# Kernel tuning notes

Measured on AMD Instinct MI355X. Metric: run time of the kernel, lower is better.

Reference implementation:

```python
import jax, jax.numpy as jnp
import numpy as np
from jax import lax


def _conv3d(x, w, b, circular=False):
    # x: (B,C,D,H,W), w: (O,I,kd,kh,kw)
    if circular:
        x = jnp.pad(x, ((0, 0), (0, 0), (1, 1), (1, 1), (1, 1)), mode='wrap')
    y = lax.conv_general_dilated(x, w, (1, 1, 1), 'VALID',
                                 dimension_numbers=('NCDHW', 'OIDHW', 'NCDHW'))
    return y + b[None, :, None, None, None]


def _inorm(x):
    # InstanceNorm3d, affine=False, eps=1e-5, biased variance over spatial dims
    mu = jnp.mean(x, axis=(2, 3, 4), keepdims=True)
    var = jnp.var(x, axis=(2, 3, 4), keepdims=True)
    return (x - mu) * lax.rsqrt(var + 1e-5)


def _gelu(x):
    return jax.nn.gelu(x, approximate=False)


def _r6_to_matrix(r6):
    eps = 1e-7
    v1 = r6[..., :3]
    v1 = v1 / (jnp.linalg.norm(v1, axis=-1, keepdims=True) + eps)
    v2 = r6[..., 3:]
    v2 = v2 - jnp.sum(v2 * v1, -1, keepdims=True) * v1
    v2 = v2 / (jnp.linalg.norm(v2, axis=-1, keepdims=True) + eps)
    v3 = jnp.cross(v1, v2)
    det = jnp.linalg.det(jnp.stack([v1, v2, v3], axis=-2))
    v3 = jnp.where(det[..., None] < 0, -v3, v3)
    return jnp.stack([v1, v2, v3], axis=-2)


def _ensure_matrix(R):
    def fnorm(v):
        return v / jnp.maximum(jnp.linalg.norm(v, axis=-1, keepdims=True), 1e-12)
    v1 = fnorm(R[..., 0, :] + 1e-6)
    v2 = R[..., 1, :]
    v2 = fnorm(v2 - jnp.sum(v2 * v1, -1, keepdims=True) * v1 + 1e-6)
    v3 = jnp.cross(v1, v2)
    det = jnp.linalg.det(jnp.stack([v1, v2, v3], axis=-2))
    v3 = jnp.where(det[..., None] < 0, -v3, v3)
    Rn = jnp.stack([v1, v2, v3], axis=-2)
    Rt = jnp.swapaxes(Rn, -2, -1)
    return 0.5 * (Rn + Rt @ Rn @ Rt)


def _rotate(X, R):
    # X: (bd, nh, L, hd); R: (nh, 3, 3). Pads hd to a multiple of 3, rotates
    # each 3-vector group by R^T-on-the-right (X_rot = X @ R^T).
    hd = X.shape[-1]
    pad = (-hd) % 3
    Xp = jnp.pad(X, ((0, 0), (0, 0), (0, 0), (0, pad))) if pad else X
    nv = Xp.shape[-1] // 3
    Xr = Xp.reshape(Xp.shape[:-1] + (nv, 3))
    Y = jnp.einsum('bhlvi,hji->bhlvj', Xr, R).reshape(Xp.shape)
    return Y[..., :hd] if pad else Y


def _forward(x, pos_emb, qkv_w, qkv_b, lp_w1, lp_b1, lp_w2, lp_b2,
             mod_w1, mod_b1, mod_w2, mod_b2, pa_w, pa_b,
             proj_w, proj_b, pos_bias_w, pos_bias_b,
             A_d, A_h, A_w, R_d, R_h, R_w, t_d, t_h, t_w):
    B, C, D, H, W = x.shape
    nh = pa_w.shape[0]
    hd = C // nh
    scale = hd ** -0.5

    # PositionalProcessing (identical for all three axial passes)
    lf = _conv3d(pos_emb, lp_w1, lp_b1, circular=True)
    lf = _conv3d(_gelu(_inorm(lf)), lp_w2, lp_b2)
    m = _conv3d(lf, mod_w1, mod_b1)
    m = jax.nn.sigmoid(_conv3d(_gelu(_inorm(m)), mod_w2, mod_b2))
    x_mod = x * m                                   # (B,C,D,H,W)
    pa = _gelu(_inorm(_conv3d(pos_emb, pa_w, pa_b)))  # (B,nh,D,H,W)

    def axial(comp, perm, inv_perm, A, R, t):
        xp = jnp.transpose(x_mod, perm)             # (B, a, b, C, L)
        Bp, a, b, _, L = xp.shape
        bd = Bp * a * b
        xf = jnp.swapaxes(xp.reshape(bd, C, L), 1, 2)  # (bd, L, C)
        qkv = (xf @ qkv_w.T + qkv_b).reshape(bd, L, 3, nh, hd)
        qkv = jnp.transpose(qkv, (2, 0, 3, 1, 4))
        q, k, v = qkv[0], qkv[1], qkv[2]
        R_qk = _r6_to_matrix(A[0].astype(jnp.float32))  # (nh,3,3), same for all bd
        R_v = _ensure_matrix(R[0])                      # (nh,3,3)
        q_r, k_r, v_r = _rotate(q, R_qk), _rotate(k, R_qk), _rotate(v, R_v)
        # axis positions: linspace on one coordinate component
        pos = jnp.zeros((L, 3), x.dtype).at[:, comp].set(jnp.linspace(-1.0, 1.0, L))
        pos_t = pos[None] + t[0]                        # (nh, L, 3)
        rel = pos_t[:, :, None, :] - pos_t[:, None, :, :]  # (nh, L, L, 3)
        bias = jnp.einsum('hqkc,c->hqk', rel, pos_bias_w[0]) + pos_bias_b[0]
        pa_p = jnp.transpose(pa, perm).reshape(bd, nh, L)
        attn = jnp.einsum('bhqd,bhkd->bhqk', q_r, k_r) * scale
        attn = jax.nn.softmax(attn + pa_p[..., None] + bias[None], axis=-1)
        out = jnp.einsum('bhqk,bhkd->bhqd', attn, v_r)
        out = jnp.transpose(out, (0, 2, 1, 3)).reshape(Bp, a, b, L, C)
        return jnp.transpose(out, inv_perm)             # back to (B,C,D,H,W)

    out = (axial(2, (0, 3, 4, 1, 2), (0, 4, 3, 1, 2), A_d, R_d, t_d)
           + axial(1, (0, 2, 4, 1, 3), (0, 4, 1, 3, 2), A_h, R_h, t_h)
           + axial(0, (0, 2, 3, 1, 4), (0, 4, 1, 2, 3), A_w, R_w, t_w))
    return jnp.einsum('oc,bcdhw->bodhw', proj_w[:, :, 0, 0, 0], out) + proj_b[None, :, None, None, None]


def setup_inputs() -> dict:
    key = jax.random.key(0)
    B, C, D, H, W, nh = 2, 128, 32, 32, 32, 8
    ks = jax.random.split(key, 24)

    def n(k, shape, s=0.05):
        return (jax.random.normal(k, shape) * s).astype(jnp.float32)

    def r6(k):
        k1, k2 = jax.random.split(k)
        v1 = jax.random.normal(k1, (1, nh, 3))
        v1 = v1 / jnp.linalg.norm(v1, axis=-1, keepdims=True)
        v2 = jax.random.normal(k2, (1, nh, 3))
        v2 = v2 - jnp.sum(v2 * v1, -1, keepdims=True) * v1
        v2 = v2 / jnp.linalg.norm(v2, axis=-1, keepdims=True)
        return jnp.concatenate([v1, v2], -1).astype(jnp.float32)

    eye = jnp.broadcast_to(jnp.eye(3, dtype=jnp.float32), (1, nh, 3, 3))
    return {
        'x': jax.random.normal(ks[0], (B, C, D, H, W), jnp.float32),
        'pos_emb': jax.random.normal(ks[1], (B, C, D, H, W), jnp.float32),
        'qkv_w': n(ks[2], (3 * C, C)), 'qkv_b': n(ks[3], (3 * C,)),
        'lp_w1': n(ks[4], (C, C, 3, 3, 3), 0.02), 'lp_b1': n(ks[5], (C,)),
        'lp_w2': n(ks[6], (C, C, 1, 1, 1)), 'lp_b2': n(ks[7], (C,)),
        'mod_w1': n(ks[8], (C, C, 1, 1, 1)), 'mod_b1': n(ks[9], (C,)),
        'mod_w2': n(ks[10], (C, C, 1, 1, 1)), 'mod_b2': n(ks[11], (C,)),
        'pa_w': n(ks[12], (nh, C, 1, 1, 1)), 'pa_b': n(ks[13], (nh,)),
        'proj_w': n(ks[14], (C, C, 1, 1, 1)), 'proj_b': n(ks[15], (C,)),
        'pos_bias_w': n(ks[16], (1, 3), 0.5), 'pos_bias_b': n(ks[17], (1,)),
        'A_d': r6(ks[18]), 'A_h': r6(ks[19]), 'A_w': r6(ks[20]),
        'R_d': eye, 'R_h': eye, 'R_w': eye,
        't_d': n(ks[21], (1, nh, 1, 3), 0.01),
        't_h': n(ks[22], (1, nh, 1, 3), 0.01),
        't_w': n(ks[23], (1, nh, 1, 3), 0.01),
    }


def reference(x, pos_emb, qkv_w, qkv_b, lp_w1, lp_b1, lp_w2, lp_b2,
              mod_w1, mod_b1, mod_w2, mod_b2, pa_w, pa_b,
              proj_w, proj_b, pos_bias_w, pos_bias_b,
              A_d, A_h, A_w, R_d, R_h, R_w, t_d, t_h, t_w):
    return _forward(x, pos_emb, qkv_w, qkv_b, lp_w1, lp_b1, lp_w2, lp_b2,
                    mod_w1, mod_b1, mod_w2, mod_b2, pa_w, pa_b,
                    proj_w, proj_b, pos_bias_w, pos_bias_b,
                    A_d, A_h, A_w, R_d, R_h, R_w, t_d, t_h, t_w)
```

## Files before the change

kernel.cpp:

```cpp
#include <hip/hip_runtime.h>
#include <cstdint>
#include <cstddef>


#define NTOK 65536
#define SPAT 32768

#define WS_R0     0ull
#define WS_A0     0ull
#define WS_A1     4194304ull
#define WS_MPREB  8388608ull
#define WS_A2     8388608ull
#define WS_XTOKB  12582912ull
#define WS_INT    16777216ull
#define WS_QKVH   20971520ull
#define WS_CONVP  33554432ull
#define WS_QKVP   33775616ull
#define WS_WCP    33800192ull
#define WS_MODW2P 33808384ull
#define WS_PROJP  33816576ull
#define WS_BC     33824768ull
#define WS_RBUF   33824896ull
#define WS_PS     33825328ull
#define WS_PSS    33956400ull
#define WS_MU1    34087472ull
#define WS_RS1    34087728ull
#define WS_MU2    34087984ull
#define WS_RS2    34088240ull

typedef __attribute__((ext_vector_type(8))) short short8;
typedef __attribute__((ext_vector_type(4))) float f32x4;
typedef __attribute__((ext_vector_type(16))) float f32x16;

__device__ __forceinline__ float gelu_f(float x) {
  return 0.5f * x * (1.0f + erff(x * 0.70710678118654752f));
}
__device__ __forceinline__ float sigmoid_f(float x) {
  return 1.0f / (1.0f + expf(-x));
}
__device__ __forceinline__ unsigned short f2bf(float x) {
  unsigned int u = __float_as_uint(x);
  unsigned int r = u + 0x7fffu + ((u >> 16) & 1u);
  return (unsigned short)(r >> 16);
}
__device__ __forceinline__ float bf2f(unsigned short u) {
  return __uint_as_float(((unsigned int)u) << 16);
}
__device__ __forceinline__ void bf16x16_load(const unsigned short* p, float* f) {
  const uint4 a = *(const uint4*)p;
  const uint4 b = *(const uint4*)(p + 8);
  const unsigned int w[8] = {a.x, a.y, a.z, a.w, b.x, b.y, b.z, b.w};
  #pragma unroll
  for (int i = 0; i < 8; ++i) {
    f[2 * i] = __uint_as_float(w[i] << 16);
    f[2 * i + 1] = __uint_as_float(w[i] & 0xffff0000u);
  }
}
__device__ __forceinline__ void gload_lds16(const void* g, void* l) {
  __builtin_amdgcn_global_load_lds(
      (const __attribute__((address_space(1))) unsigned int*)g,
      (__attribute__((address_space(3))) unsigned int*)l, 16, 0, 0);
}
__device__ __forceinline__ float dot3(const float* a, const float* b) {
  return a[0] * b[0] + a[1] * b[1] + a[2] * b[2];
}
__device__ __forceinline__ void cross3(const float* a, const float* b, float* c) {
  c[0] = a[1] * b[2] - a[2] * b[1];
  c[1] = a[2] * b[0] - a[0] * b[2];
  c[2] = a[0] * b[1] - a[1] * b[0];
}

__device__ void r6_to_matrix(const float* r6, float* R) {
  float v1[3] = {r6[0], r6[1], r6[2]};
  float n1 = sqrtf(dot3(v1, v1));
  float inv1 = 1.0f / (n1 + 1e-7f);
  v1[0] *= inv1; v1[1] *= inv1; v1[2] *= inv1;
  float v2[3] = {r6[3], r6[4], r6[5]};
  float d = dot3(v2, v1);
  v2[0] -= d * v1[0]; v2[1] -= d * v1[1]; v2[2] -= d * v1[2];
  float n2 = sqrtf(dot3(v2, v2));
  float inv2 = 1.0f / (n2 + 1e-7f);
  v2[0] *= inv2; v2[1] *= inv2; v2[2] *= inv2;
  float v3[3]; cross3(v1, v2, v3);
  float cx[3]; cross3(v2, v3, cx);
  float det = dot3(v1, cx);
  if (det < 0.0f) { v3[0] = -v3[0]; v3[1] = -v3[1]; v3[2] = -v3[2]; }
  R[0] = v1[0]; R[1] = v1[1]; R[2] = v1[2];
  R[3] = v2[0]; R[4] = v2[1]; R[5] = v2[2];
  R[6] = v3[0]; R[7] = v3[1]; R[8] = v3[2];
}

__device__ void ensure_matrix(const float* Rin, float* Ro) {
  float a[3] = {Rin[0] + 1e-6f, Rin[1] + 1e-6f, Rin[2] + 1e-6f};
  float na = fmaxf(sqrtf(dot3(a, a)), 1e-12f);
  float v1[3] = {a[0] / na, a[1] / na, a[2] / na};
  float b0[3] = {Rin[3], Rin[4], Rin[5]};
  float d = dot3(b0, v1);
  float bb[3] = {b0[0] - d * v1[0] + 1e-6f, b0[1] - d * v1[1] + 1e-6f, b0[2] - d * v1[2] + 1e-6f};
  float nb = fmaxf(sqrtf(dot3(bb, bb)), 1e-12f);
  float v2[3] = {bb[0] / nb, bb[1] / nb, bb[2] / nb};
  float v3[3]; cross3(v1, v2, v3);
  float cx[3]; cross3(v2, v3, cx);
  float det = dot3(v1, cx);
  if (det < 0.0f) { v3[0] = -v3[0]; v3[1] = -v3[1]; v3[2] = -v3[2]; }
  float Rn[9] = {v1[0], v1[1], v1[2], v2[0], v2[1], v2[2], v3[0], v3[1], v3[2]};
  float T1[9], T2[9];
  for (int i = 0; i < 3; ++i)
    for (int j = 0; j < 3; ++j) {
      float s = 0.f;
      for (int k = 0; k < 3; ++k) s += Rn[k * 3 + i] * Rn[k * 3 + j];
      T1[i * 3 + j] = s;
    }
  for (int i = 0; i < 3; ++i)
    for (int j = 0; j < 3; ++j) {
      float s = 0.f;
      for (int k = 0; k < 3; ++k) s += T1[i * 3 + k] * Rn[j * 3 + k];
      T2[i * 3 + j] = s;
    }
  for (int i = 0; i < 9; ++i) Ro[i] = 0.5f * (Rn[i] + T2[i]);
}

__device__ __forceinline__ void rot16(const float* R, const float* x, float* y) {
  #pragma unroll
  for (int g = 0; g < 5; ++g) {
    float a = x[3 * g], b = x[3 * g + 1], c = x[3 * g + 2];
    y[3 * g + 0] = R[0] * a + R[1] * b + R[2] * c;
    y[3 * g + 1] = R[3] * a + R[4] * b + R[5] * c;
    y[3 * g + 2] = R[6] * a + R[7] * b + R[8] * c;
  }
  y[15] = R[0] * x[15];
}

__global__ __launch_bounds__(256) void prep_transpose_kernel(
    const float* __restrict__ lp_w1, const float* __restrict__ qkv_w,
    const float* __restrict__ mod_w1, const float* __restrict__ lp_w2,
    const float* __restrict__ lp_b2, const float* __restrict__ mod_b1,
    const float* __restrict__ mod_w2, const float* __restrict__ proj_w,
    const float* __restrict__ Ad, const float* __restrict__ Ah,
    const float* __restrict__ Aw, const float* __restrict__ Rd,
    const float* __restrict__ Rh, const float* __restrict__ Rw,
    const float* __restrict__ x, const float* __restrict__ pe,
    unsigned short* __restrict__ convP, unsigned short* __restrict__ qkvP,
    unsigned short* __restrict__ WcP, unsigned short* __restrict__ modw2P,
    unsigned short* __restrict__ projP, float* __restrict__ bc,
    float* __restrict__ Rbuf, unsigned short* __restrict__ xtokb,
    unsigned short* __restrict__ inT) {
  __shared__ float lds[32][132];
  if (blockIdx.x < 256) {
    int gid = blockIdx.x * 256 + threadIdx.x;
    for (int f = gid; f < 442368; f += 65536) {
      int e = f & 7;
      int co = (f >> 3) & 127;
      int rest = f >> 10;
      int l4 = rest & 3;
      int ks = (rest >> 2) & 3;
      int dxt = rest >> 4;
      int dx = dxt % 3;
      int tap = dxt / 3;
      int dz = tap / 3, dy = tap % 3;
      int ci = ks * 32 + l4 * 8 + e;
      convP[f] = f2bf(lp_w1[(co * 128 + ci) * 27 + dz * 9 + dy * 3 + dx]);
    }
    if (gid < 49152) qkvP[gid] = f2bf(qkv_w[gid]);
    if (gid < 16384) {
      modw2P[gid] = f2bf(mod_w2[gid]);
      projP[gid] = f2bf(proj_w[gid]);
      int o = gid >> 7, i = gid & 127;
      float s = 0.f;
      for (int c = 0; c < 128; ++c) s += mod_w1[o * 128 + c] * lp_w2[c * 128 + i];
      WcP[gid] = f2bf(s);
    }
    if (gid < 128) {
      float s = 0.f;
      for (int c = 0; c < 128; ++c) s += mod_w1[gid * 128 + c] * lp_b2[c];
      bc[gid] = s + mod_b1[gid];
    }
    if (blockIdx.x == 0 && threadIdx.x >= 224 && threadIdx.x < 248) {
      int tid = threadIdx.x - 224;
      int ax = tid >> 3, h = tid & 7;
      const float* A = (ax == 0) ? Ad : ((ax == 1) ? Ah : Aw);
      const float* R = (ax == 0) ? Rd : ((ax == 1) ? Rh : Rw);
      float Rq[9], Rv[9];
      r6_to_matrix(A + h * 6, Rq);
      ensure_matrix(R + h * 9, Rv);
      float* dst = Rbuf + (ax * 8 + h) * 18;
      for (int i = 0; i < 9; ++i) { dst[i] = Rq[i]; dst[9 + i] = Rv[i]; }
    }
    return;
  }
  int blk = blockIdx.x - 256;
  int b = blk >> 10;
  int dh = blk & 1023;
  int tid = threadIdx.x;
  size_t planebase = ((size_t)b << 22) + ((size_t)dh << 5);
  size_t tb = ((size_t)blk) << 5;
  #pragma unroll
  for (int r = 0; r < 16; ++r) {
    int idx = r * 256 + tid;
    int ci = idx >> 5, w = idx & 31;
    lds[w][ci] = x[planebase + ((size_t)ci << 15) + w];
  }
  __syncthreads();
  #pragma unroll
  for (int r = 0; r < 16; ++r) {
    int idx = r * 256 + tid;
    int w = idx >> 7, ci = idx & 127;
    xtokb[(tb + w) * 128 + ci] = f2bf(lds[w][ci]);
  }
  __syncthreads();
  #pragma unroll
  for (int r = 0; r < 16; ++r) {
    int idx = r * 256 + tid;
    int ci = idx >> 5, w = idx & 31;
    lds[w][ci] = pe[planebase + ((size_t)ci << 15) + w];
  }
  __syncthreads();
  #pragma unroll
  for (int r = 0; r < 16; ++r) {
    int idx = r * 256 + tid;
    int w = idx >> 7, ci = idx & 127;
    inT[(tb + w) * 128 + ci] = f2bf(lds[w][ci]);
  }
}

__global__ __launch_bounds__(256, 4) void conv_mfma_kernel(
    const unsigned short* __restrict__ inT, const unsigned short* __restrict__ Bp,
    const float* __restrict__ b1, unsigned short* __restrict__ out,
    float* __restrict__ ps, float* __restrict__ pss) {
  __shared__ unsigned short Als[16384];
  __shared__ float sumb[128];
  __shared__ float sqb[128];
  const int orig = blockIdx.x;
  const int blk = ((orig & 7) << 7) + (orig >> 3);
  const int b = blk >> 9, d = (blk >> 4) & 31, hg = blk & 15;
  const int h0 = hg << 1;
  const int tid = threadIdx.x;
  const int lane = tid & 63;
  const int wid = tid >> 6;
  const int l15 = lane & 15, l4 = lane >> 4;

  f32x4 acc[4][2];
  #pragma unroll
  for (int mt = 0; mt < 4; ++mt)
    #pragma unroll
    for (int nt = 0; nt < 2; ++nt)
      #pragma unroll
      for (int r = 0; r < 4; ++r) acc[mt][nt][r] = 0.f;

  int mw[4], mhh[4];
  #pragma unroll
  for (int mt = 0; mt < 4; ++mt) {
    int m = mt * 16 + l15;
    mhh[mt] = m >> 5;
    mw[mt] = m & 31;
  }
  const size_t tokbase = ((size_t)b << 15) + ((size_t)d << 10) + ((size_t)h0 << 5);

  auto stage = [&](int dz) {
    const int zr = (d + dz + 31) & 31;
    #pragma unroll
    for (int p = 0; p < 8; ++p) {
      const int g = p * 256 + tid;
      const int tok = g >> 4, gi = g & 15;
      const int r = tok >> 5, w = tok & 31;
      const int yr = (h0 + r + 31) & 31;
      const size_t srcbyte = ((((size_t)b << 15) + ((size_t)zr << 10) + ((size_t)yr << 5) + w) << 8)
                             + (size_t)((gi ^ (w & 7)) << 4);
      gload_lds16((const char*)inT + srcbyte, (char*)Als + (size_t)g * 16);
    }
  };

  auto compute = [&](int dz) {
    #pragma unroll
    for (int dy = 0; dy < 3; ++dy) {
      const int tap = dz * 3 + dy;
      #pragma unroll
      for (int dx = 0; dx < 3; ++dx) {
        int abase[4], asw[4];
        #pragma unroll
        for (int mt = 0; mt < 4; ++mt) {
          const int wsft = (mw[mt] + dx + 31) & 31;
          const int stok = (mhh[mt] + dy) * 32 + wsft;
          abase[mt] = stok * 256;
          asw[mt] = (wsft & 7) << 4;
        }
        #pragma unroll
        for (int ks = 0; ks < 4; ++ks) {
          const int k2 = (ks * 32 + l4 * 8) * 2;
          const int bbase = (((tap * 3 + dx) * 4 + ks) * 4 + l4) * 1024;
          short8 afr[4], bfr[2];
          #pragma unroll
          for (int nt = 0; nt < 2; ++nt) {
            const int co = wid * 32 + nt * 16 + l15;
            bfr[nt] = *(const short8*)(Bp + bbase + co * 8);
          }
          #pragma unroll
          for (int mt = 0; mt < 4; ++mt)
            afr[mt] = *(const short8*)((const char*)Als + abase[mt] + (k2 ^ asw[mt]));
          __builtin_amdgcn_s_setprio(1);
          #pragma unroll
          for (int mt = 0; mt < 4; ++mt)
            #pragma unroll
            for (int nt = 0; nt < 2; ++nt)
              acc[mt][nt] = __builtin_amdgcn_mfma_f32_16x16x32_bf16(afr[mt], bfr[nt],
                                                                    acc[mt][nt], 0, 0, 0);
          __builtin_amdgcn_s_setprio(0);
        }
      }
    }
  };

  for (int dz = 0; dz < 3; ++dz) {
    stage(dz);
    __syncthreads();
    compute(dz);
    if (dz < 2) __syncthreads();
  }

  #pragma unroll
  for (int nt = 0; nt < 2; ++nt) {
    const int co = wid * 32 + nt * 16 + l15;
    const float bias = b1[co];
    float s = 0.f, q = 0.f;
    #pragma unroll
    for (int mt = 0; mt < 4; ++mt) {
      #pragma unroll
      for (int r = 0; r < 4; ++r) {
        const int m = mt * 16 + l4 * 4 + r;
        const float v = acc[mt][nt][r] + bias;
        out[(tokbase + m) * 128 + co] = f2bf(v);
        s += v; q += v * v;
      }
    }
    s += __shfl_xor(s, 16); s += __shfl_xor(s, 32);
    q += __shfl_xor(q, 16); q += __shfl_xor(q, 32);
    if (l4 == 0) { sumb[co] = s; sqb[co] = q; }
  }
  __syncthreads();
  if (tid < 128) {
    ps[blk * 128 + tid] = sumb[tid];
    pss[blk * 128 + tid] = sqb[tid];
  }
}

__global__ __launch_bounds__(64) void stats_final_kernel(
    const float* __restrict__ ps, const float* __restrict__ pss,
    float* __restrict__ mu, float* __restrict__ rs, int nb) {
  const int pair = blockIdx.x;
  const int b = pair >> 7, c = pair & 127;
  const int lane = threadIdx.x;
  float s = 0.f, ss = 0.f;
  for (int j = lane; j < nb; j += 64) {
    const int idx = ((b * nb + j) << 7) + c;
    s += ps[idx];
    ss += pss[idx];
  }
  #pragma unroll
  for (int o = 32; o > 0; o >>= 1) {
    s += __shfl_xor(s, o);
    ss += __shfl_xor(ss, o);
  }
  if (lane == 0) {
    float m = s * (1.0f / 32768.0f);
    float v = ss * (1.0f / 32768.0f) - m * m;
    mu[pair] = m;
    rs[pair] = rsqrtf(v + 1e-5f);
  }
}

template <int PRE, int AB16, int POST, int STATS>
__global__ __launch_bounds__(256) void gemm_mfma_kernel(
    const void* __restrict__ Avoid, const unsigned short* __restrict__ Wp,
    const float* __restrict__ bias, void* __restrict__ Yvoid, int O,
    const float* __restrict__ mu, const float* __restrict__ rs,
    const unsigned short* __restrict__ xtb, float* __restrict__ ps,
    float* __restrict__ pss) {
  __shared__ float sumb[128][2];
  __shared__ float sqb[128][2];
  const int tid = threadIdx.x;
  const int lane = tid & 63, wid = tid >> 6;
  const int wm = wid >> 1, wn = wid & 1;
  const int l15 = lane & 15, l4 = lane >> 4;
  const int og = blockIdx.x * 128;
  const int t0 = blockIdx.y * 128;
  const int bidx = t0 >> 15;
  const float* Af = (const float*)Avoid;
  const unsigned short* Ab = (const unsigned short*)Avoid;
  float* Yf = (float*)Yvoid;
  unsigned short* Yb = (unsigned short*)Yvoid;

  f32x4 acc[4][4];
  #pragma unroll
  for (int mt = 0; mt < 4; ++mt)
    #pragma unroll
    for (int nt = 0; nt < 4; ++nt)
      #pragma unroll
      for (int r = 0; r < 4; ++r) acc[mt][nt][r] = 0.f;

  #pragma unroll
  for (int ks = 0; ks < 4; ++ks) {
    const int kb = ks * 32 + l4 * 8;
    short8 a[4], bfr[4];
    float4 m0, m1, r0, r1;
    if constexpr (PRE == 1) {
      m0 = *(const float4*)(mu + bidx * 128 + kb);
      m1 = *(const float4*)(mu + bidx * 128 + kb + 4);
      r0 = *(const float4*)(rs + bidx * 128 + kb);
      r1 = *(const float4*)(rs + bidx * 128 + kb + 4);
    }
    #pragma unroll
    for (int mt = 0; mt < 4; ++mt) {
      const int tok = t0 + wm * 64 + mt * 16 + l15;
      float v[16];
      bool have = false;
      if constexpr (AB16 == 1) {
        if constexpr (PRE == 1) {
          bf16x16_load(Ab + (size_t)tok * 128 + kb, v);
          have = true;
        } else {
          a[mt] = *(const short8*)(Ab + (size_t)tok * 128 + kb);
        }
      } else {
        const float* ap = Af + (size_t)tok * 128 + kb;
        float4 v0 = *(const float4*)ap;
        float4 v1 = *(const float4*)(ap + 4);
        v[0] = v0.x; v[1] = v0.y; v[2] = v0.z; v[3] = v0.w;
        v[4] = v1.x; v[5] = v1.y; v[6] = v1.z; v[7] = v1.w;
        have = true;
      }
      if (have) {
        if constexpr (PRE == 1) {
          const float mm[8] = {m0.x, m0.y, m0.z, m0.w, m1.x, m1.y, m1.z, m1.w};
          const float rr[8] = {r0.x, r0.y, r0.z, r0.w, r1.x, r1.y, r1.z, r1.w};
          #pragma unroll
          for (int j = 0; j < 8; ++j) v[j] = gelu_f((v[j] - mm[j]) * rr[j]);
        }
        short8 t;
        #pragma unroll
        for (int j = 0; j < 8; ++j) t[j] = (short)f2bf(v[j]);
        a[mt] = t;
      }
    }
    #pragma unroll
    for (int nt = 0; nt < 4; ++nt) {
      const int o = og + wn * 64 + nt * 16 + l15;
      bfr[nt] = *(const short8*)(Wp + (size_t)o * 128 + kb);
    }
    #pragma unroll
    for (int mt = 0; mt < 4; ++mt)
      #pragma unroll
      for (int nt = 0; nt < 4; ++nt)
        acc[mt][nt] = __builtin_amdgcn_mfma_f32_16x16x32_bf16(a[mt], bfr[nt], acc[mt][nt], 0, 0, 0);
  }

  #pragma unroll
  for (int nt = 0; nt < 4; ++nt) {
    const int o = og + wn * 64 + nt * 16 + l15;
    const float bb = bias[o];
    float s = 0.f, q = 0.f;
    #pragma unroll
    for (int mt = 0; mt < 4; ++mt) {
      #pragma unroll
      for (int r = 0; r < 4; ++r) {
        const int t = t0 + wm * 64 + mt * 16 + l4 * 4 + r;
        const float v = acc[mt][nt][r] + bb;
        if constexpr (POST == 0) {
          Yf[(size_t)t * O + o] = v;
        } else if constexpr (POST == 2) {
          Yb[(size_t)t * O + o] = f2bf(v);
        }
        if constexpr (STATS) { s += v; q += v * v; }
      }
    }
    if constexpr (STATS) {
      s += __shfl_xor(s, 16); s += __shfl_xor(s, 32);
      q += __shfl_xor(q, 16); q += __shfl_xor(q, 32);
      if (l4 == 0) { sumb[o - og][wm] = s; sqb[o - og][wm] = q; }
    }
  }
  if constexpr (STATS) {
    __syncthreads();
    if (tid < 128) {
      ps[blockIdx.y * 128 + tid] = sumb[tid][0] + sumb[tid][1];
      pss[blockIdx.y * 128 + tid] = sqb[tid][0] + sqb[tid][1];
    }
  }
}

__global__ __launch_bounds__(256) void gateqkv_mfma_kernel(
    const unsigned short* __restrict__ mpreb, const unsigned short* __restrict__ modw2P,
    const float* __restrict__ mod_b2, const unsigned short* __restrict__ xtb,
    const unsigned short* __restrict__ qkvP, const float* __restrict__ qkv_b,
    unsigned short* __restrict__ qkvt, const float* __restrict__ mu,
    const float* __restrict__ rs) {
  __shared__ char xm[32768];
  const int tid = threadIdx.x;
  const int lane = tid & 63, wid = tid >> 6;
  const int wm = wid >> 1, wn = wid & 1;
  const int l15 = lane & 15, l4 = lane >> 4;
  const int t0 = blockIdx.x * 128;
  const int bidx = t0 >> 15;

  f32x4 acc[4][4];
  #pragma unroll
  for (int mt = 0; mt < 4; ++mt)
    #pragma unroll
    for (int nt = 0; nt < 4; ++nt)
      #pragma unroll
      for (int r = 0; r < 4; ++r) acc[mt][nt][r] = 0.f;

  #pragma unroll
  for (int ks = 0; ks < 4; ++ks) {
    const int kb = ks * 32 + l4 * 8;
    short8 a[4], bfr[4];
    const float4 m0 = *(const float4*)(mu + bidx * 128 + kb);
    const float4 m1 = *(const float4*)(mu + bidx * 128 + kb + 4);
    const float4 r0 = *(const float4*)(rs + bidx * 128 + kb);
    const float4 r1 = *(const float4*)(rs + bidx * 128 + kb + 4);
    const float mm[8] = {m0.x, m0.y, m0.z, m0.w, m1.x, m1.y, m1.z, m1.w};
    const float rr[8] = {r0.x, r0.y, r0.z, r0.w, r1.x, r1.y, r1.z, r1.w};
    #pragma unroll
    for (int mt = 0; mt < 4; ++mt) {
      const int tok = t0 + wm * 64 + mt * 16 + l15;
      float v[16];
      bf16x16_load(mpreb + (size_t)tok * 128 + kb, v);
      short8 t;
      #pragma unroll
      for (int j = 0; j < 8; ++j) t[j] = (short)f2bf(gelu_f((v[j] - mm[j]) * rr[j]));
      a[mt] = t;
    }
    #pragma unroll
    for (int nt = 0; nt < 4; ++nt) {
      const int o = wn * 64 + nt * 16 + l15;
      bfr[nt] = *(const short8*)(modw2P + (size_t)o * 128 + kb);
    }
    #pragma unroll
    for (int mt = 0; mt < 4; ++mt)
      #pragma unroll
      for (int nt = 0; nt < 4; ++nt)
        acc[mt][nt] = __builtin_amdgcn_mfma_f32_16x16x32_bf16(a[mt], bfr[nt], acc[mt][nt], 0, 0, 0);
  }
  #pragma unroll
  for (int nt = 0; nt < 4; ++nt) {
    const int o = wn * 64 + nt * 16 + l15;
    const float bb = mod_b2[o];
    #pragma unroll
    for (int mt = 0; mt < 4; ++mt) {
      #pragma unroll
      for (int r = 0; r < 4; ++r) {
        const int tl = wm * 64 + mt * 16 + l4 * 4 + r;
        const int t = t0 + tl;
        const float v = sigmoid_f(acc[mt][nt][r] + bb) * bf2f(xtb[(size_t)t * 128 + o]);
        *(unsigned short*)(xm + tl * 256 + ((o * 2) ^ ((tl & 7) << 4))) = f2bf(v);
      }
    }
  }
  __syncthreads();

  for (int c = 0; c < 3; ++c) {
    #pragma unroll
    for (int mt = 0; mt < 4; ++mt)
      #pragma unroll
      for (int nt = 0; nt < 4; ++nt)
        #pragma unroll
        for (int r = 0; r < 4; ++r) acc[mt][nt][r] = 0.f;
    #pragma unroll
    for (int ks = 0; ks < 4; ++ks) {
      const int kb = ks * 32 + l4 * 8;
      short8 a[4], bfr[4];
      #pragma unroll
      for (int mt = 0; mt < 4; ++mt) {
        const int tl = wm * 64 + mt * 16 + l15;
        a[mt] = *(const short8*)(xm + tl * 256 + ((kb * 2) ^ ((tl & 7) << 4)));
      }
      #pragma unroll
      for (int nt = 0; nt < 4; ++nt) {
        const int o = c * 128 + wn * 64 + nt * 16 + l15;
        bfr[nt] = *(const short8*)(qkvP + (size_t)o * 128 + kb);
      }
      #pragma unroll
      for (int mt = 0; mt < 4; ++mt)
        #pragma unroll
        for (int nt = 0; nt < 4; ++nt)
          acc[mt][nt] = __builtin_amdgcn_mfma_f32_16x16x32_bf16(a[mt], bfr[nt], acc[mt][nt], 0, 0, 0);
    }
    #pragma unroll
    for (int nt = 0; nt < 4; ++nt) {
      const int o = c * 128 + wn * 64 + nt * 16 + l15;
      const float bb = qkv_b[o];
      const int hsub = (o & 127) >> 4, ch = o & 15;
      #pragma unroll
      for (int mt = 0; mt < 4; ++mt) {
        #pragma unroll
        for (int r = 0; r < 4; ++r) {
          const int t = t0 + wm * 64 + mt * 16 + l4 * 4 + r;
          qkvt[(size_t)t * 384 + hsub * 48 + c * 16 + ch] = f2bf(acc[mt][nt][r] + bb);
        }
      }
    }
  }
}

__global__ __launch_bounds__(256) void proj_mfma_kernel(
    const unsigned short* __restrict__ A0b, const unsigned short* __restrict__ A1b,
    const unsigned short* __restrict__ A2b, const unsigned short* __restrict__ Wp,
    const float* __restrict__ bias, float* __restrict__ out) {
  const int tid = threadIdx.x;
  const int lane = tid & 63, wid = tid >> 6;
  const int wm = wid >> 1, wn = wid & 1;
  const int l15 = lane & 15, l4 = lane >> 4;
  const int t0 = blockIdx.x * 128;

  f32x4 acc[4][4];
  #pragma unroll
  for (int mt = 0; mt < 4; ++mt)
    #pragma unroll
    for (int nt = 0; nt < 4; ++nt)
      #pragma unroll
      for (int r = 0; r < 4; ++r) acc[mt][nt][r] = 0.f;

  #pragma unroll
  for (int ks = 0; ks < 4; ++ks) {
    const int kb = ks * 32 + l4 * 8;
    short8 a[4], bfr[4];
    #pragma unroll
    for (int mt = 0; mt < 4; ++mt) {
      const int o = wm * 64 + mt * 16 + l15;
      a[mt] = *(const short8*)(Wp + (size_t)o * 128 + kb);
    }
    #pragma unroll
    for (int nt = 0; nt < 4; ++nt) {
      const int tok = t0 + wn * 64 + nt * 16 + l15;
      const size_t off = (size_t)tok * 128 + kb;
      short8 s0 = *(const short8*)(A0b + off);
      short8 s1 = *(const short8*)(A1b + off);
      short8 s2 = *(const short8*)(A2b + off);
      short8 r;
      #pragma unroll
      for (int i = 0; i < 8; ++i) {
        float f = bf2f((unsigned short)s0[i]) + bf2f((unsigned short)s1[i]) +
                  bf2f((unsigned short)s2[i]);
        r[i] = (short)f2bf(f);
      }
      bfr[nt] = r;
    }
    #pragma unroll
    for (int mt = 0; mt < 4; ++mt)
      #pragma unroll
      for (int nt = 0; nt < 4; ++nt)
        acc[mt][nt] = __builtin_amdgcn_mfma_f32_16x16x32_bf16(a[mt], bfr[nt], acc[mt][nt], 0, 0, 0);
  }

  #pragma unroll
  for (int nt = 0; nt < 4; ++nt) {
    const int tok = t0 + wn * 64 + nt * 16 + l15;
    const int dhw = tok & 32767, bB = tok >> 15;
    #pragma unroll
    for (int mt = 0; mt < 4; ++mt) {
      #pragma unroll
      for (int r = 0; r < 4; ++r) {
        const int o = wm * 64 + mt * 16 + l4 * 4 + r;
        out[((size_t)(bB * 128 + o) << 15) + dhw] = acc[mt][nt][r] + bias[o];
      }
    }
  }
}

__global__ __launch_bounds__(512) void attn_mfma_kernel(
    const unsigned short* __restrict__ qkvt, const float* __restrict__ Rbuf,
    const float* __restrict__ pbw, unsigned short* __restrict__ a0,
    unsigned short* __restrict__ a1, unsigned short* __restrict__ a2) {
  __shared__ unsigned short rows[32 * 392];
  __shared__ unsigned short Vt[8][16 * 40];
  __shared__ float Ot[8][32 * 20];
  const int axial = blockIdx.y;
  const int seq = blockIdx.x;
  unsigned short* dstbuf = (axial == 0) ? a0 : ((axial == 1) ? a1 : a2);
  const int tid = threadIdx.x;
  const int lane = tid & 63, head = tid >> 6;
  const int tok = lane & 31, hi = lane >> 5;
  const int b = seq >> 10, rem = seq & 1023;
  const int u = rem >> 5, v = rem & 31;
  int base, stride, comp;
  if (axial == 0)      { base = (b << 15) + (u << 5) + v;         stride = 1024; comp = 2; }
  else if (axial == 1) { base = (b << 15) + (u << 10) + v;        stride = 32;   comp = 1; }
  else                 { base = (b << 15) + (u << 10) + (v << 5); stride = 1;    comp = 0; }

  #pragma unroll
  for (int p = 0; p < 3; ++p) {
    const int c = p * 512 + tid;
    const int r = c / 48, cw = c - r * 48;
    const size_t src = ((size_t)base + (size_t)r * stride) * 384 + (size_t)cw * 8;
    *(uint4*)((char*)rows + r * 784 + cw * 16) = *(const uint4*)(qkvt + src);
  }
  __syncthreads();

  const float* Rp = Rbuf + (axial * 8 + head) * 18;
  const float rq00 = fabsf(Rp[0]);
  const unsigned short* myrow = rows + tok * 392 + head * 48;
  short8 aq = *(const short8*)(myrow + hi * 8);
  short8 ak = *(const short8*)(myrow + 16 + hi * 8);
  short8 av = *(const short8*)(myrow + 32 + hi * 8);
  if (hi) {
    aq[7] = (short)f2bf(bf2f((unsigned short)aq[7]) * rq00);
    ak[7] = (short)f2bf(bf2f((unsigned short)ak[7]) * rq00);
  }
  #pragma unroll
  for (int e = 0; e < 8; ++e) Vt[head][(hi * 8 + e) * 40 + tok] = (unsigned short)av[e];

  f32x16 sacc;
  #pragma unroll
  for (int r = 0; r < 16; ++r) sacc[r] = 0.f;
  sacc = __builtin_amdgcn_mfma_f32_32x32x16_bf16(ak, aq, sacc, 0, 0, 0);
  const float wb = pbw[comp];
  float p[16];
  float mmax = -1e30f;
  #pragma unroll
  for (int r = 0; r < 16; ++r) {
    const int kk = (r & 3) + 4 * hi + 8 * (r >> 2);
    const float lin = -1.0f + (2.0f / 31.0f) * (float)kk;
    p[r] = sacc[r] * 0.25f - lin * wb;
    mmax = fmaxf(mmax, p[r]);
  }
  mmax = fmaxf(mmax, __shfl_xor(mmax, 32));
  float sum = 0.f;
  #pragma unroll
  for (int r = 0; r < 16; ++r) { p[r] = expf(p[r] - mmax); sum += p[r]; }
  sum += __shfl_xor(sum, 32);
  const float inv = 1.0f / sum;
  #pragma unroll
  for (int r = 0; r < 16; ++r) p[r] *= inv;
  unsigned pk[8], sw[8];
  #pragma unroll
  for (int j = 0; j < 8; ++j) {
    unsigned r_;
    asm("v_cvt_pk_bf16_f32 %0, %1, %2" : "=v"(r_) : "v"(p[2 * j]), "v"(p[2 * j + 1]));
    pk[j] = r_;
  }
  #pragma unroll
  for (int j = 0; j < 8; ++j) sw[j] = (unsigned)__shfl_xor((int)pk[j], 32);
  uint4 Fu, Gu;
  Fu.x = hi ? sw[2] : pk[0];
  Fu.y = hi ? sw[3] : pk[1];
  Fu.z = hi ? pk[2] : sw[0];
  Fu.w = hi ? pk[3] : sw[1];
  Gu.x = hi ? sw[6] : pk[4];
  Gu.y = hi ? sw[7] : pk[5];
  Gu.z = hi ? pk[6] : sw[4];
  Gu.w = hi ? pk[7] : sw[5];
  short8 Pf = *(short8*)&Fu;
  short8 Pg = *(short8*)&Gu;
  const unsigned short* vrow = Vt[head] + (tok & 15) * 40;
  short8 Bv0 = *(const short8*)(vrow + hi * 8);
  short8 Bv1 = *(const short8*)(vrow + 16 + hi * 8);
  f32x16 oacc;
  #pragma unroll
  for (int r = 0; r < 16; ++r) oacc[r] = 0.f;
  oacc = __builtin_amdgcn_mfma_f32_32x32x16_bf16(Pf, Bv0, oacc, 0, 0, 0);
  oacc = __builtin_amdgcn_mfma_f32_32x32x16_bf16(Pg, Bv1, oacc, 0, 0, 0);
  if (tok < 16) {
    #pragma unroll
    for (int r = 0; r < 16; ++r) {
      const int q = (r & 3) + 4 * hi + 8 * (r >> 2);
      Ot[head][q * 20 + tok] = oacc[r];
    }
  }
  if (lane < 32) {
    float o16[16], y16[16], Rv[9];
    #pragma unroll
    for (int j = 0; j < 16; ++j) o16[j] = Ot[head][lane * 20 + j];
    #pragma unroll
    for (int i = 0; i < 9; ++i) Rv[i] = Rp[9 + i];
    rot16(Rv, o16, y16);
    unsigned outw[8];
    #pragma unroll
    for (int j = 0; j < 8; ++j)
      outw[j] = ((unsigned)f2bf(y16[2 * j + 1]) << 16) | (unsigned)f2bf(y16[2 * j]);
    const size_t t2 = (size_t)base + (size_t)lane * stride;
    unsigned short* dst = dstbuf + t2 * 128 + head * 16;
    uint4 o0 = {outw[0], outw[1], outw[2], outw[3]};
    uint4 o1 = {outw[4], outw[5], outw[6], outw[7]};
    *(uint4*)dst = o0;
    *(uint4*)(dst + 8) = o1;
  }
}

extern "C" void kernel_launch(void* const* d_in, const int* in_sizes, int n_in,
                              void* d_out, int out_size, void* d_ws, size_t ws_size,
                              hipStream_t stream) {
  const float* x       = (const float*)d_in[0];
  const float* pos_emb = (const float*)d_in[1];
  const float* qkv_w   = (const float*)d_in[2];
  const float* qkv_b   = (const float*)d_in[3];
  const float* lp_w1   = (const float*)d_in[4];
  const float* lp_b1   = (const float*)d_in[5];
  const float* lp_w2   = (const float*)d_in[6];
  const float* lp_b2   = (const float*)d_in[7];
  const float* mod_w1  = (const float*)d_in[8];
  const float* mod_b1  = (const float*)d_in[9];
  const float* mod_w2  = (const float*)d_in[10];
  const float* mod_b2  = (const float*)d_in[11];
  const float* proj_w  = (const float*)d_in[14];
  const float* proj_b  = (const float*)d_in[15];
  const float* pbw     = (const float*)d_in[16];
  const float* Ad      = (const float*)d_in[18];
  const float* Ah      = (const float*)d_in[19];
  const float* Aw      = (const float*)d_in[20];
  const float* Rd      = (const float*)d_in[21];
  const float* Rh      = (const float*)d_in[22];
  const float* Rw      = (const float*)d_in[23];

  float* ws = (float*)d_ws;
  unsigned short* lfb    = (unsigned short*)(ws + WS_R0);
  unsigned short* A0b    = (unsigned short*)(ws + WS_A0);
  unsigned short* A1b    = (unsigned short*)(ws + WS_A1);
  unsigned short* A2b    = (unsigned short*)(ws + WS_A2);
  unsigned short* mpreb  = (unsigned short*)(ws + WS_MPREB);
  unsigned short* xtokb  = (unsigned short*)(ws + WS_XTOKB);
  unsigned short* inT    = (unsigned short*)(ws + WS_INT);
  unsigned short* qkvt   = (unsigned short*)(ws + WS_QKVH);
  unsigned short* convP  = (unsigned short*)(ws + WS_CONVP);
  unsigned short* qkvP   = (unsigned short*)(ws + WS_QKVP);
  unsigned short* WcP    = (unsigned short*)(ws + WS_WCP);
  unsigned short* modw2P = (unsigned short*)(ws + WS_MODW2P);
  unsigned short* projP  = (unsigned short*)(ws + WS_PROJP);
  float* bc     = ws + WS_BC;
  float* Rbuf   = ws + WS_RBUF;
  float* ps     = ws + WS_PS;
  float* pss    = ws + WS_PSS;
  float* mu1    = ws + WS_MU1;
  float* rs1    = ws + WS_RS1;
  float* mu2    = ws + WS_MU2;
  float* rs2    = ws + WS_RS2;

  prep_transpose_kernel<<<2304, 256, 0, stream>>>(
      lp_w1, qkv_w, mod_w1, lp_w2, lp_b2, mod_b1, mod_w2, proj_w,
      Ad, Ah, Aw, Rd, Rh, Rw, x, pos_emb,
      convP, qkvP, WcP, modw2P, projP, bc, Rbuf, xtokb, inT);
  conv_mfma_kernel<<<1024, 256, 0, stream>>>(inT, convP, lp_b1, lfb, ps, pss);
  stats_final_kernel<<<256, 64, 0, stream>>>(ps, pss, mu1, rs1, 512);
  gemm_mfma_kernel<1, 1, 2, 1><<<dim3(1, 512), 256, 0, stream>>>(
      lfb, WcP, bc, mpreb, 128, mu1, rs1, nullptr, ps, pss);
  stats_final_kernel<<<256, 64, 0, stream>>>(ps, pss, mu2, rs2, 256);
  gateqkv_mfma_kernel<<<512, 256, 0, stream>>>(
      mpreb, modw2P, mod_b2, xtokb, qkvP, qkv_b, qkvt, mu2, rs2);
  attn_mfma_kernel<<<dim3(2048, 3), 512, 0, stream>>>(qkvt, Rbuf, pbw, A0b, A1b, A2b);
  proj_mfma_kernel<<<512, 256, 0, stream>>>(A0b, A1b, A2b, projP, proj_b, (float*)d_out);
}
```

Before: 251.0 us.

## Use tanh-approx GELU, fast exp, and precompute GELU tile in LDS once

Replaces exact erf-based GELU with the tanh approximation computed via __expf, and swaps expf for __expf in sigmoid. In the gate/QKV kernel, the normalize+GELU of the input tile is now computed once per block into a swizzled LDS buffer instead of redundantly by both N-waves, then read back as MFMA A fragments. This cuts duplicated transcendental work and global loads, at the cost of 32KB extra LDS (lower occupancy) and a numerical deviation from exact GELU.

```diff
diff --git a/kernel.cpp b/kernel.cpp
--- a/kernel.cpp
+++ b/kernel.cpp
@@ -33,10 +33,14 @@
 typedef __attribute__((ext_vector_type(16))) float f32x16;
 
 __device__ __forceinline__ float gelu_f(float x) {
-  return 0.5f * x * (1.0f + erff(x * 0.70710678118654752f));
+  float u = 0.79788456080286536f * (x + 0.044715f * x * x * x);
+  u = fminf(u, 40.0f);
+  float e = __expf(2.0f * u);
+  float t = (e - 1.0f) / (e + 1.0f);
+  return 0.5f * x * (1.0f + t);
 }
 __device__ __forceinline__ float sigmoid_f(float x) {
-  return 1.0f / (1.0f + expf(-x));
+  return 1.0f / (1.0f + __expf(-x));
 }
 __device__ __forceinline__ unsigned short f2bf(float x) {
   unsigned int u = __float_as_uint(x);
@@ -52,6 +56,15 @@
   const unsigned int w[8] = {a.x, a.y, a.z, a.w, b.x, b.y, b.z, b.w};
   #pragma unroll
   for (int i = 0; i < 8; ++i) {
+    f[2 * i] = __uint_as_float(w[i] << 16);
+    f[2 * i + 1] = __uint_as_float(w[i] & 0xffff0000u);
+  }
+}
+__device__ __forceinline__ void bf16x8_load(const unsigned short* p, float* f) {
+  const uint4 a = *(const uint4*)p;
+  const unsigned int w[4] = {a.x, a.y, a.z, a.w};
+  #pragma unroll
+  for (int i = 0; i < 4; ++i) {
     f[2 * i] = __uint_as_float(w[i] << 16);
     f[2 * i + 1] = __uint_as_float(w[i] & 0xffff0000u);
   }
@@ -493,6 +506,7 @@
     const unsigned short* __restrict__ qkvP, const float* __restrict__ qkv_b,
     unsigned short* __restrict__ qkvt, const float* __restrict__ mu,
     const float* __restrict__ rs) {
+  __shared__ char ga[32768];
   __shared__ char xm[32768];
   const int tid = threadIdx.x;
   const int lane = tid & 63, wid = tid >> 6;
@@ -501,6 +515,26 @@
   const int t0 = blockIdx.x * 128;
   const int bidx = t0 >> 15;
 
+  #pragma unroll
+  for (int r = 0; r < 8; ++r) {
+    const int c = r * 256 + tid;
+    const int tl = c >> 4;
+    const int kc = (c & 15) * 8;
+    float v[8];
+    bf16x8_load(mpreb + (size_t)(t0 + tl) * 128 + kc, v);
+    const float4 m0 = *(const float4*)(mu + bidx * 128 + kc);
+    const float4 m1 = *(const float4*)(mu + bidx * 128 + kc + 4);
+    const float4 r0 = *(const float4*)(rs + bidx * 128 + kc);
+    const float4 r1 = *(const float4*)(rs + bidx * 128 + kc + 4);
+    const float mm[8] = {m0.x, m0.y, m0.z, m0.w, m1.x, m1.y, m1.z, m1.w};
+    const float rr[8] = {r0.x, r0.y, r0.z, r0.w, r1.x, r1.y, r1.z, r1.w};
+    short8 t;
+    #pragma unroll
+    for (int j = 0; j < 8; ++j) t[j] = (short)f2bf(gelu_f((v[j] - mm[j]) * rr[j]));
+    *(short8*)(ga + tl * 256 + ((kc * 2) ^ ((tl & 7) << 4))) = t;
+  }
+  __syncthreads();
+
   f32x4 acc[4][4];
   #pragma unroll
   for (int mt = 0; mt < 4; ++mt)
@@ -513,21 +547,10 @@
   for (int ks = 0; ks < 4; ++ks) {
     const int kb = ks * 32 + l4 * 8;
     short8 a[4], bfr[4];
-    const float4 m0 = *(const float4*)(mu + bidx * 128 + kb);
-    const float4 m1 = *(const float4*)(mu + bidx * 128 + kb + 4);
-    const float4 r0 = *(const float4*)(rs + bidx * 128 + kb);
-    const float4 r1 = *(const float4*)(rs + bidx * 128 + kb + 4);
-    const float mm[8] = {m0.x, m0.y, m0.z, m0.w, m1.x, m1.y, m1.z, m1.w};
-    const float rr[8] = {r0.x, r0.y, r0.z, r0.w, r1.x, r1.y, r1.z, r1.w};
     #pragma unroll
     for (int mt = 0; mt < 4; ++mt) {
-      const int tok = t0 + wm * 64 + mt * 16 + l15;
-      float v[16];
-      bf16x16_load(mpreb + (size_t)tok * 128 + kb, v);
-      short8 t;
-      #pragma unroll
-      for (int j = 0; j < 8; ++j) t[j] = (short)f2bf(gelu_f((v[j] - mm[j]) * rr[j]));
-      a[mt] = t;
+      const int tl = wm * 64 + mt * 16 + l15;
+      a[mt] = *(const short8*)(ga + tl * 256 + ((kb * 2) ^ ((tl & 7) << 4)));
     }
     #pragma unroll
     for (int nt = 0; nt < 4; ++nt) {
```

New measurement: 228.0 us. -9.2%, faster.
